# Kernel optimization log

Hardware: AMD Instinct MI355X
Metric: run time of the kernel (lower is better)

## Reference

```python
import jax, jax.numpy as jnp
import numpy as np

B, T, C = 4, 2048, 1024
H = 16
D = C // H  # 64

def setup_inputs() -> dict:
    key = jax.random.key(0)
    k1, k2, k3, k4, k5 = jax.random.split(key, 5)
    s = 0.02
    return {
        "x": jax.random.normal(k1, (B, T, C), dtype=jnp.float32),
        "Wqkv": jax.random.normal(k2, (C, 3 * C), dtype=jnp.float32) * s,
        "bqkv": jnp.zeros((3 * C,), dtype=jnp.float32),
        "Wout": jax.random.normal(k3, (C, C), dtype=jnp.float32) * s,
        "bout": jnp.zeros((C,), dtype=jnp.float32),
    }

def reference(x, Wqkv, bqkv, Wout, bout):
    b, t, c = x.shape
    scale = D ** -0.5
    qkv = x @ Wqkv + bqkv                      # [B,T,3C]
    qkv = qkv.reshape(b, t, 3, H, D)
    q = qkv[:, :, 0].transpose(0, 2, 1, 3)     # [B,H,T,D]
    k = qkv[:, :, 1].transpose(0, 2, 1, 3)
    v = qkv[:, :, 2].transpose(0, 2, 1, 3)
    att = jnp.einsum('bhqd,bhkd->bhqk', q, k) * scale
    causal = jnp.tril(jnp.ones((t, t), dtype=bool))
    att = jnp.where(causal, att, -jnp.inf)
    att = jax.nn.softmax(att, axis=-1)
    y = jnp.einsum('bhqk,bhkd->bhqd', att, v)  # [B,H,T,D]
    y = y.transpose(0, 2, 1, 3).reshape(b, t, c)
    return y @ Wout + bout
```

## Files before the change

### kernel.cpp

```cpp
#include <hip/hip_runtime.h>
#include <hip/hip_bf16.h>


using f32x4 = __attribute__((ext_vector_type(4))) float;
using s16x8 = __attribute__((ext_vector_type(8))) short;
using s16x4 = __attribute__((ext_vector_type(4))) short;

#define MFMA16(a, b, c) __builtin_amdgcn_mfma_f32_16x16x32_bf16(a, b, c, 0, 0, 0)

__device__ __forceinline__ unsigned short f2bf(float f) {
    unsigned u = __builtin_bit_cast(unsigned, f);
    u += 0x7fffu + ((u >> 16) & 1u);
    return (unsigned short)(u >> 16);
}

__device__ __forceinline__ void gl_lds16(const void* g, void* l) {
    __builtin_amdgcn_global_load_lds(
        (const __attribute__((address_space(1))) void*)g,
        (__attribute__((address_space(3))) void*)l, 16, 0, 0);
}

__global__ __launch_bounds__(256) void cvt_x(const float* __restrict__ x,
                                             unsigned short* __restrict__ xb, int n4) {
    int i = blockIdx.x * 256 + threadIdx.x;
    if (i < n4) {
        f32x4 v = ((const f32x4*)x)[i];
        s16x4 o;
        o[0] = (short)f2bf(v[0]); o[1] = (short)f2bf(v[1]);
        o[2] = (short)f2bf(v[2]); o[3] = (short)f2bf(v[3]);
        ((s16x4*)xb)[i] = o;
    }
}

__global__ __launch_bounds__(256) void cvt_tr(const float* __restrict__ W,
                                              unsigned short* __restrict__ Wt,
                                              int R, int Cc) {
    __shared__ unsigned short tile[64][72];
    const int r0 = blockIdx.x * 64, c0 = blockIdx.y * 64;
    const int tid = threadIdx.x;
    const int r = tid >> 4, c4 = (tid & 15) * 4;
#pragma unroll
    for (int i = 0; i < 4; ++i) {
        f32x4 v = *(const f32x4*)(W + (size_t)(r0 + r + i * 16) * Cc + c0 + c4);
#pragma unroll
        for (int j = 0; j < 4; ++j) tile[r + i * 16][c4 + j] = f2bf(v[j]);
    }
    __syncthreads();
#pragma unroll
    for (int i = 0; i < 4; ++i) {
        s16x4 o;
#pragma unroll
        for (int j = 0; j < 4; ++j) o[j] = (short)tile[c4 + j][r + i * 16];
        *(s16x4*)(Wt + (size_t)(c0 + r + i * 16) * R + r0 + c4) = o;
    }
}

template <int MODE>
__global__ __launch_bounds__(256, 2) void gemm_bt(
    const unsigned short* __restrict__ A, const unsigned short* __restrict__ Bt,
    const float* __restrict__ bias,
    unsigned short* __restrict__ qp, unsigned short* __restrict__ kp,
    unsigned short* __restrict__ vtp, float* __restrict__ outp,
    int M, int N, int K)
{
    __shared__ unsigned short As[2][128 * 64];
    __shared__ unsigned short Bs[2][128 * 64];

    const int tid  = threadIdx.x;
    const int lane = tid & 63, w = tid >> 6;
    const int wm = w >> 1, wn = w & 1;
    const int g = lane >> 4, li = lane & 15;
    const int m0 = blockIdx.x * 128, n0 = blockIdx.y * 128;

    const int srow = lane >> 3;
    const int ssw  = ((lane & 7) ^ srow) * 8;

    f32x4 acc[4][4] = {};

    auto STAGE = [&](int buf, int k0) {
#pragma unroll
        for (int j = 0; j < 4; ++j) {
            const int rr = w * 32 + j * 8;
            gl_lds16(A  + (size_t)(m0 + rr + srow) * K + k0 + ssw, &As[buf][rr * 64]);
            gl_lds16(Bt + (size_t)(n0 + rr + srow) * K + k0 + ssw, &Bs[buf][rr * 64]);
        }
    };

    STAGE(0, 0);
    asm volatile("s_waitcnt vmcnt(0)" ::: "memory");
    __syncthreads();

    const int nt = K >> 6;
    int cur = 0;
    for (int t = 0; t < nt; ++t) {
        if (t + 1 < nt) STAGE(cur ^ 1, (t + 1) << 6);

        s16x8 af[4][2], bf[4][2];
#pragma unroll
        for (int i = 0; i < 4; ++i) {
            const int ra = wm * 64 + i * 16 + li;
            const int rb = wn * 64 + i * 16 + li;
#pragma unroll
            for (int kk = 0; kk < 2; ++kk) {
                af[i][kk] = *(const s16x8*)(
                    &As[cur][ra * 64 + (((kk * 4 + g) ^ (ra & 7)) << 3)]);
                bf[i][kk] = *(const s16x8*)(
                    &Bs[cur][rb * 64 + (((kk * 4 + g) ^ (rb & 7)) << 3)]);
            }
        }

        __builtin_amdgcn_s_setprio(1);
#pragma unroll
        for (int kk = 0; kk < 2; ++kk)
#pragma unroll
            for (int mi = 0; mi < 4; ++mi)
#pragma unroll
                for (int ni = 0; ni < 4; ++ni)
                    acc[mi][ni] = MFMA16(af[mi][kk], bf[ni][kk], acc[mi][ni]);
        __builtin_amdgcn_s_setprio(0);

        asm volatile("s_waitcnt vmcnt(0)" ::: "memory");
        __syncthreads();
        cur ^= 1;
    }

#pragma unroll
    for (int ni = 0; ni < 4; ++ni) {
        const int n = n0 + wn * 64 + ni * 16 + li;
        const float bv = bias[n];
        const int s = n >> 10, h = (n >> 6) & 15, d = n & 63;
#pragma unroll
        for (int mi = 0; mi < 4; ++mi) {
            const int mB = m0 + wm * 64 + mi * 16 + g * 4;
            float v0 = acc[mi][ni][0] + bv, v1 = acc[mi][ni][1] + bv;
            float v2 = acc[mi][ni][2] + bv, v3 = acc[mi][ni][3] + bv;
            if (MODE == 0) {
                const int b = mB >> 11, tt = mB & 2047;
                if (s == 2) {
                    unsigned pk01, pk23;
                    asm("v_cvt_pk_bf16_f32 %0, %1, %2" : "=v"(pk01) : "v"(v0), "v"(v1));
                    asm("v_cvt_pk_bf16_f32 %0, %1, %2" : "=v"(pk23) : "v"(v2), "v"(v3));
                    unsigned short* dst = vtp + ((size_t)(b * 16 + h) * 64 + d) * 2048 + tt;
                    *(unsigned*)dst = pk01;
                    *(unsigned*)(dst + 2) = pk23;
                } else {
                    const float sc2 = (s == 0) ? 0.1803368801111143f : 1.0f;
                    unsigned short* dst =
                        ((s == 0) ? qp : kp) + ((size_t)(b * 16 + h) * 2048 + tt) * 64 + d;
                    dst[0]   = f2bf(v0 * sc2);
                    dst[64]  = f2bf(v1 * sc2);
                    dst[128] = f2bf(v2 * sc2);
                    dst[192] = f2bf(v3 * sc2);
                }
            } else {
                float* dst = outp + (size_t)mB * N + n;
                dst[0] = v0; dst[N] = v1; dst[2 * N] = v2; dst[3 * N] = v3;
            }
        }
    }
}

__device__ __forceinline__ void stage_load(
    const unsigned short* __restrict__ kb, const unsigned short* __restrict__ vtb,
    int kbase, int w, int lane, s16x8 (&kr)[2], s16x8 (&vr)[2])
{
    const int srow = lane >> 3;
    const int sw = ((lane & 7) ^ srow) * 8;
#pragma unroll
    for (int jj = 0; jj < 2; ++jj) {
        const int row = (w * 2 + jj) * 8 + srow;
        kr[jj] = *(const s16x8*)(kb + (size_t)(kbase + row) * 64 + sw);
        vr[jj] = *(const s16x8*)(vtb + (size_t)row * 2048 + kbase + sw);
    }
}

__device__ __forceinline__ void stage_write(
    unsigned short* Ks, unsigned short* Vs, int w, int lane,
    const s16x8 (&kr)[2], const s16x8 (&vr)[2])
{
#pragma unroll
    for (int jj = 0; jj < 2; ++jj) {
        const int j = w * 2 + jj;
        *(s16x8*)(Ks + j * 512 + lane * 8) = kr[jj];
        *(s16x8*)(Vs + j * 512 + lane * 8) = vr[jj];
    }
}

__device__ __forceinline__ void qk_softmax(
    const unsigned short* Ks, const s16x8 qf0, const s16x8 qf1,
    f32x4 (&O)[4], float& m, float& l,
    unsigned short (*Psw)[72], s16x8& pf0, s16x8& pf1,
    int kbase, int wq0, int qrow, int g, int li)
{
    f32x4 sT[4];
    __builtin_amdgcn_s_setprio(1);
#pragma unroll
    for (int nf = 0; nf < 4; ++nf) {
        const int r = nf * 16 + li;
        s16x8 kf0 = *(const s16x8*)(Ks + r * 64 + ((g ^ (li & 7)) << 3));
        s16x8 kf1 = *(const s16x8*)(Ks + r * 64 + (((g + 4) ^ (li & 7)) << 3));
        f32x4 a = {};
        a = MFMA16(kf0, qf0, a);
        a = MFMA16(kf1, qf1, a);
        sT[nf] = a;
    }
    __builtin_amdgcn_s_setprio(0);

    if (kbase + 63 > wq0) {
#pragma unroll
        for (int nf = 0; nf < 4; ++nf)
#pragma unroll
            for (int r = 0; r < 4; ++r)
                if (kbase + nf * 16 + g * 4 + r > qrow) sT[nf][r] = -1e30f;
    }

    float t0 = fmaxf(fmaxf(sT[0][0], sT[0][1]), sT[0][2]);
    float t1 = fmaxf(fmaxf(sT[0][3], sT[1][0]), sT[1][1]);
    float t2 = fmaxf(fmaxf(sT[1][2], sT[1][3]), sT[2][0]);
    float t3 = fmaxf(fmaxf(sT[2][1], sT[2][2]), sT[2][3]);
    float t4 = fmaxf(fmaxf(sT[3][0], sT[3][1]), sT[3][2]);
    float mx = fmaxf(fmaxf(t0, t1), t2);
    mx = fmaxf(fmaxf(mx, t3), fmaxf(t4, sT[3][3]));
    mx = fmaxf(mx, __shfl_xor(mx, 16));
    mx = fmaxf(mx, __shfl_xor(mx, 32));

    if (__any(mx > m + 8.f)) {
        const float mnew = fmaxf(m, mx);
        const float fac  = __builtin_amdgcn_exp2f(m - mnew);
        m = mnew;
        l *= fac;
        float facr[4];
#pragma unroll
        for (int r = 0; r < 4; ++r) facr[r] = __shfl(fac, g * 4 + r);
#pragma unroll
        for (int nf = 0; nf < 4; ++nf)
#pragma unroll
            for (int r = 0; r < 4; ++r) O[nf][r] *= facr[r];
    }

    float rs = 0.f;
#pragma unroll
    for (int nf = 0; nf < 4; ++nf)
#pragma unroll
        for (int r = 0; r < 4; ++r) {
            float p = __builtin_amdgcn_exp2f(sT[nf][r] - m);
            sT[nf][r] = p;
            rs += p;
        }
    rs += __shfl_xor(rs, 16);
    rs += __shfl_xor(rs, 32);
    l += rs;

#pragma unroll
    for (int nf = 0; nf < 4; ++nf) {
        unsigned pk0, pk1;
        asm("v_cvt_pk_bf16_f32 %0, %1, %2" : "=v"(pk0) : "v"(sT[nf][0]), "v"(sT[nf][1]));
        asm("v_cvt_pk_bf16_f32 %0, %1, %2" : "=v"(pk1) : "v"(sT[nf][2]), "v"(sT[nf][3]));
        uint2 pv; pv.x = pk0; pv.y = pk1;
        *(uint2*)(&Psw[li][nf * 16 + g * 4]) = pv;
    }
    pf0 = *(const s16x8*)(&Psw[li][g * 8]);
    pf1 = *(const s16x8*)(&Psw[li][32 + g * 8]);
}

__global__ __launch_bounds__(256, 4) void attn_k(
    const unsigned short* __restrict__ qbuf,
    const unsigned short* __restrict__ kbuf,
    const unsigned short* __restrict__ vtbuf,
    unsigned short* __restrict__ ybuf)
{
    __shared__ unsigned short Ks[4096];
    __shared__ unsigned short Vs[4096];
    __shared__ unsigned short Ps[4][16][72];

    const int tid  = threadIdx.x;
    const int lane = tid & 63, w = tid >> 6;
    const int g = lane >> 4, li = lane & 15;

    const int id   = blockIdx.x;
    const int slot = id >> 3;
    const int bh   = (id & 7) * 8 + (slot & 7);
    const int bx   = slot >> 3;
    const int qtA  = 31 - bx, qtB = bx;

    const unsigned short* qb  = qbuf  + (size_t)bh * 131072;
    const unsigned short* kb  = kbuf  + (size_t)bh * 131072;
    const unsigned short* vtb = vtbuf + (size_t)bh * 131072;
    const int b = bh >> 4, h = bh & 15;

    const int wqA = qtA * 64 + w * 16, qrowA = wqA + li;
    const int wqB = qtB * 64 + w * 16, qrowB = wqB + li;

    const unsigned short* qrA = qb + (size_t)qrowA * 64 + g * 8;
    const s16x8 qfA0 = *(const s16x8*)qrA;
    const s16x8 qfA1 = *(const s16x8*)(qrA + 32);
    const unsigned short* qrB = qb + (size_t)qrowB * 64 + g * 8;
    const s16x8 qfB0 = *(const s16x8*)qrB;
    const s16x8 qfB1 = *(const s16x8*)(qrB + 32);

    f32x4 OA[4] = {}, OB[4] = {};
    float mA = -1e30f, lA = 0.f, mB = -1e30f, lB = 0.f;

    const int nkb = qtA + 1;
    s16x8 kr[2], vr[2];
    stage_load(kb, vtb, 0, w, lane, kr, vr);
    stage_write(Ks, Vs, w, lane, kr, vr);
    __syncthreads();

    for (int t = 0; t < nkb; ++t) {
        const int kbase = t * 64;
        const bool actB = (t <= qtB);
        const bool more = (t + 1 < nkb);

        if (more) stage_load(kb, vtb, kbase + 64, w, lane, kr, vr);

        s16x8 pfA0, pfA1, pfB0, pfB1;
        qk_softmax(Ks, qfA0, qfA1, OA, mA, lA, &Ps[w][0], pfA0, pfA1,
                   kbase, wqA, qrowA, g, li);
        if (actB)
            qk_softmax(Ks, qfB0, qfB1, OB, mB, lB, &Ps[w][0], pfB0, pfB1,
                       kbase, wqB, qrowB, g, li);

        __builtin_amdgcn_s_setprio(1);
#pragma unroll
        for (int nf = 0; nf < 4; ++nf) {
            const int d = nf * 16 + li;
            s16x8 vf0 = *(const s16x8*)(Vs + d * 64 + ((g ^ (li & 7)) << 3));
            s16x8 vf1 = *(const s16x8*)(Vs + d * 64 + (((g + 4) ^ (li & 7)) << 3));
            OA[nf] = MFMA16(pfA0, vf0, OA[nf]);
            OA[nf] = MFMA16(pfA1, vf1, OA[nf]);
            if (actB) {
                OB[nf] = MFMA16(pfB0, vf0, OB[nf]);
                OB[nf] = MFMA16(pfB1, vf1, OB[nf]);
            }
        }
        __builtin_amdgcn_s_setprio(0);

        if (more) {
            __syncthreads();
            stage_write(Ks, Vs, w, lane, kr, vr);
            __syncthreads();
        }
    }

    {
        const float linv = __builtin_amdgcn_rcpf(lA);
        float lr[4];
#pragma unroll
        for (int r = 0; r < 4; ++r) lr[r] = __shfl(linv, g * 4 + r);
#pragma unroll
        for (int nf = 0; nf < 4; ++nf)
#pragma unroll
            for (int r = 0; r < 4; ++r) {
                const int row = wqA + g * 4 + r;
                ybuf[((size_t)(b * 2048 + row)) * 1024 + h * 64 + nf * 16 + li] =
                    f2bf(OA[nf][r] * lr[r]);
            }
    }
    {
        const float linv = __builtin_amdgcn_rcpf(lB);
        float lr[4];
#pragma unroll
        for (int r = 0; r < 4; ++r) lr[r] = __shfl(linv, g * 4 + r);
#pragma unroll
        for (int nf = 0; nf < 4; ++nf)
#pragma unroll
            for (int r = 0; r < 4; ++r) {
                const int row = wqB + g * 4 + r;
                ybuf[((size_t)(b * 2048 + row)) * 1024 + h * 64 + nf * 16 + li] =
                    f2bf(OB[nf][r] * lr[r]);
            }
    }
}

extern "C" void kernel_launch(void* const* d_in, const int* in_sizes, int n_in,
                              void* d_out, int out_size, void* d_ws, size_t ws_size,
                              hipStream_t stream)
{
    const float* x    = (const float*)d_in[0];
    const float* Wqkv = (const float*)d_in[1];
    const float* bqkv = (const float*)d_in[2];
    const float* Wout = (const float*)d_in[3];
    const float* bout = (const float*)d_in[4];

    unsigned short* ws0 = (unsigned short*)d_ws;
    unsigned short* ws1 = ws0 + (size_t)8388608;
    unsigned short* ws2 = ws0 + (size_t)2 * 8388608;
    unsigned short* ws3 = ws0 + (size_t)3 * 8388608;

    unsigned short* xbf   = (unsigned short*)d_out;
    unsigned short* WqkvT = xbf + (size_t)8388608;

    cvt_x<<<8192, 256, 0, stream>>>(x, xbf, 2097152);
    cvt_tr<<<dim3(16, 48), 256, 0, stream>>>(Wqkv, WqkvT, 1024, 3072);
    gemm_bt<0><<<dim3(64, 24), 256, 0, stream>>>(
        xbf, WqkvT, bqkv, ws0, ws1, ws2, nullptr, 8192, 3072, 1024);
    attn_k<<<1024, 256, 0, stream>>>(ws0, ws1, ws2, ws3);
    cvt_tr<<<dim3(16, 16), 256, 0, stream>>>(Wout, ws0, 1024, 1024);
    gemm_bt<1><<<dim3(64, 8), 256, 0, stream>>>(
        ws3, ws0, bout, nullptr, nullptr, nullptr, (float*)d_out, 8192, 1024, 1024);
}
```

Before: 178.3 us.

## Use async global-to-LDS loads with finer vmcnt waits in GEMM and attention

```diff
diff --git a/kernel.cpp b/kernel.cpp
--- a/kernel.cpp
+++ b/kernel.cpp
@@ -19,6 +19,9 @@
         (const __attribute__((address_space(1))) void*)g,
         (__attribute__((address_space(3))) void*)l, 16, 0, 0);
 }
+
+#define VMCNT(N) asm volatile("s_waitcnt vmcnt(" #N ")" ::: "memory")
+#define RBAR()   __builtin_amdgcn_s_barrier()
 
 __global__ __launch_bounds__(256) void cvt_x(const float* __restrict__ x,
                                              unsigned short* __restrict__ xb, int n4) {
@@ -87,13 +90,17 @@
     };
 
     STAGE(0, 0);
-    asm volatile("s_waitcnt vmcnt(0)" ::: "memory");
-    __syncthreads();
 
     const int nt = K >> 6;
     int cur = 0;
     for (int t = 0; t < nt; ++t) {
-        if (t + 1 < nt) STAGE(cur ^ 1, (t + 1) << 6);
+        if (t + 1 < nt) {
+            STAGE(cur ^ 1, (t + 1) << 6);
+            VMCNT(8);
+        } else {
+            VMCNT(0);
+        }
+        RBAR();
 
         s16x8 af[4][2], bf[4][2];
 #pragma unroll
@@ -119,8 +126,7 @@
                     acc[mi][ni] = MFMA16(af[mi][kk], bf[ni][kk], acc[mi][ni]);
         __builtin_amdgcn_s_setprio(0);
 
-        asm volatile("s_waitcnt vmcnt(0)" ::: "memory");
-        __syncthreads();
+        RBAR();
         cur ^= 1;
     }
 
@@ -160,32 +166,6 @@
     }
 }
 
-__device__ __forceinline__ void stage_load(
-    const unsigned short* __restrict__ kb, const unsigned short* __restrict__ vtb,
-    int kbase, int w, int lane, s16x8 (&kr)[2], s16x8 (&vr)[2])
-{
-    const int srow = lane >> 3;
-    const int sw = ((lane & 7) ^ srow) * 8;
-#pragma unroll
-    for (int jj = 0; jj < 2; ++jj) {
-        const int row = (w * 2 + jj) * 8 + srow;
-        kr[jj] = *(const s16x8*)(kb + (size_t)(kbase + row) * 64 + sw);
-        vr[jj] = *(const s16x8*)(vtb + (size_t)row * 2048 + kbase + sw);
-    }
-}
-
-__device__ __forceinline__ void stage_write(
-    unsigned short* Ks, unsigned short* Vs, int w, int lane,
-    const s16x8 (&kr)[2], const s16x8 (&vr)[2])
-{
-#pragma unroll
-    for (int jj = 0; jj < 2; ++jj) {
-        const int j = w * 2 + jj;
-        *(s16x8*)(Ks + j * 512 + lane * 8) = kr[jj];
-        *(s16x8*)(Vs + j * 512 + lane * 8) = vr[jj];
-    }
-}
-
 __device__ __forceinline__ void qk_softmax(
     const unsigned short* Ks, const s16x8 qf0, const s16x8 qf1,
     f32x4 (&O)[4], float& m, float& l,
@@ -269,7 +249,7 @@
     const unsigned short* __restrict__ vtbuf,
     unsigned short* __restrict__ ybuf)
 {
-    __shared__ unsigned short Ks[4096];
+    __shared__ unsigned short Ks[2][4096];
     __shared__ unsigned short Vs[4096];
     __shared__ unsigned short Ps[4][16][72];
 
@@ -287,6 +267,24 @@
     const unsigned short* kb  = kbuf  + (size_t)bh * 131072;
     const unsigned short* vtb = vtbuf + (size_t)bh * 131072;
     const int b = bh >> 4, h = bh & 15;
+
+    const int srow = lane >> 3;
+    const int ssw  = ((lane & 7) ^ srow) * 8;
+
+    auto STAGE_K = [&](int buf, int kbase) {
+#pragma unroll
+        for (int jj = 0; jj < 2; ++jj) {
+            const int j = w * 2 + jj, row = j * 8 + srow;
+            gl_lds16(kb + (size_t)(kbase + row) * 64 + ssw, &Ks[buf][j * 512]);
+        }
+    };
+    auto STAGE_V = [&](int kbase) {
+#pragma unroll
+        for (int jj = 0; jj < 2; ++jj) {
+            const int j = w * 2 + jj, row = j * 8 + srow;
+            gl_lds16(vtb + (size_t)row * 2048 + kbase + ssw, &Vs[j * 512]);
+        }
+    };
 
     const int wqA = qtA * 64 + w * 16, qrowA = wqA + li;
     const int wqB = qtB * 64 + w * 16, qrowB = wqB + li;
@@ -302,24 +300,34 @@
     float mA = -1e30f, lA = 0.f, mB = -1e30f, lB = 0.f;
 
     const int nkb = qtA + 1;
-    s16x8 kr[2], vr[2];
-    stage_load(kb, vtb, 0, w, lane, kr, vr);
-    stage_write(Ks, Vs, w, lane, kr, vr);
-    __syncthreads();
-
+    STAGE_K(0, 0);
+    STAGE_V(0);
+    VMCNT(0);
+    RBAR();
+
+    int bK = 0;
     for (int t = 0; t < nkb; ++t) {
         const int kbase = t * 64;
         const bool actB = (t <= qtB);
         const bool more = (t + 1 < nkb);
 
-        if (more) stage_load(kb, vtb, kbase + 64, w, lane, kr, vr);
+        if (more) {
+            STAGE_K(bK ^ 1, kbase + 64);
+            VMCNT(4);
+        } else {
+            VMCNT(2);
+        }
+        RBAR();
 
         s16x8 pfA0, pfA1, pfB0, pfB1;
-        qk_softmax(Ks, qfA0, qfA1, OA, mA, lA, &Ps[w][0], pfA0, pfA1,
+        qk_softmax(&Ks[bK][0], qfA0, qfA1, OA, mA, lA, &Ps[w][0], pfA0, pfA1,
                    kbase, wqA, qrowA, g, li);
         if (actB)
-            qk_softmax(Ks, qfB0, qfB1, OB, mB, lB, &Ps[w][0], pfB0, pfB1,
+            qk_softmax(&Ks[bK][0], qfB0, qfB1, OB, mB, lB, &Ps[w][0], pfB0, pfB1,
                        kbase, wqB, qrowB, g, li);
+
+        if (more) VMCNT(2); else VMCNT(0);
+        RBAR();
 
         __builtin_amdgcn_s_setprio(1);
 #pragma unroll
@@ -337,10 +345,10 @@
         __builtin_amdgcn_s_setprio(0);
 
         if (more) {
-            __syncthreads();
-            stage_write(Ks, Vs, w, lane, kr, vr);
-            __syncthreads();
-        }
+            RBAR();
+            STAGE_V(kbase + 64);
+        }
+        bK ^= 1;
     }
 
     {
```

Measured after the change: 165.2 us. 7.4% less time.
